# Performance work log

Hardware: AMD Instinct MI355X
Metric: run time of the kernel (lower is better)

Reference implementation:

```python
import jax, jax.numpy as jnp
import numpy as np

B, P, N, S = 32, 16384, 64, 5
BOX_W, SCALE_W, CTX_W, CONF_W = 2.0, 1.0, 1.5, 1.0
BETA = 0.1
REG = 0.1


def _box_iou(a, b):
    # a: [P,4], b: [N,4], boxes are (x1,y1,x2,y2) (torchvision box_iou)
    area_a = (a[:, 2] - a[:, 0]) * (a[:, 3] - a[:, 1])
    area_b = (b[:, 2] - b[:, 0]) * (b[:, 3] - b[:, 1])
    lt = jnp.maximum(a[:, None, :2], b[None, :, :2])
    rb = jnp.minimum(a[:, None, 2:], b[None, :, 2:])
    wh = jnp.maximum(rb - lt, 0.0)
    inter = wh[..., 0] * wh[..., 1]
    return inter / (area_a[:, None] + area_b[None, :] - inter)


def _smooth_l1(x, y, beta=BETA):
    d = jnp.abs(x - y)
    return jnp.where(d < beta, 0.5 * d * d / beta, d - 0.5 * beta)


def _bce_logits(x, y):
    # numerically stable BCEWithLogits, matches torch
    return jnp.maximum(x, 0.0) - x * y + jnp.log1p(jnp.exp(-jnp.abs(x)))


def _per_batch(pscore, pbox, pscale, pctx, tbox, tscale, tctx):
    ious = _box_iou(pbox, tbox)                      # [P, N]
    best_ious = ious.max(axis=0)                     # [N]
    best_idx = ious.argmax(axis=0)                   # [N]
    valid = best_ious > 0.5
    nv = valid.sum()
    denom = jnp.maximum(nv, 1).astype(pbox.dtype)

    # SmoothL1 box loss, weighted by matched IoU, masked mean over valid rows
    sl1 = _smooth_l1(pbox[best_idx], tbox)                          # [N,4]
    box_l = (sl1 * best_ious[:, None] * valid[:, None]).sum() / (denom * 4.0)

    # CrossEntropy over scale classes for matched anchors
    logp = jax.nn.log_softmax(pscale[best_idx], axis=-1)            # [N,S]
    ce = -jnp.take_along_axis(logp, tscale[:, None].astype(jnp.int32), axis=1)[:, 0]
    scale_l = (ce * valid).sum() / denom

    # BCEWithLogits context loss for matched anchors
    bce = _bce_logits(pctx[best_idx], tctx)
    ctx_l = (bce * valid).sum() / denom

    # confidence targets: scatter best IoUs into a zero vector at matched anchors
    Pn = pscore.shape[0]
    idx_safe = jnp.where(valid, best_idx, Pn)
    conf_target = jnp.zeros((Pn + 1,), pscore.dtype).at[idx_safe].max(
        jnp.where(valid, best_ious, 0.0))[:Pn]
    conf_l = _bce_logits(pscore, conf_target).mean()

    # fallback regularization branch (taken when no IoU > 0.5)
    box_reg = jnp.abs(pbox).mean()
    safe = jnp.where(pscale + 1e-6 > 0, pscale + 1e-6, 1.0)
    scale_reg = -(pscale * jnp.log(safe)).mean()
    ctx_reg = jax.nn.softplus(pctx).mean()    # BCEWithLogits vs zeros
    conf_reg = jax.nn.softplus(pscore).mean()

    any_v = nv > 0
    return (jnp.where(any_v, box_l, REG * box_reg),
            jnp.where(any_v, scale_l, REG * scale_reg),
            jnp.where(any_v, ctx_l, REG * ctx_reg),
            jnp.where(any_v, conf_l, conf_reg))


def _forward(pred_scores, pred_boxes, pred_scales, pred_context,
             target_boxes, target_scales, target_context):
    bl, sl, cl, fl = jax.vmap(_per_batch)(
        pred_scores, pred_boxes, pred_scales, pred_context,
        target_boxes, target_scales, target_context)
    box_loss = BOX_W * bl.mean()
    scale_loss = SCALE_W * sl.mean()
    ctx_loss = CTX_W * cl.mean()
    conf_loss = CONF_W * fl.mean()
    total = box_loss + scale_loss + ctx_loss + conf_loss
    return total, box_loss, scale_loss, ctx_loss, conf_loss


def setup_inputs() -> dict:
    key = jax.random.key(0)
    ks = jax.random.split(key, 9)

    def rand_boxes(k, shape):
        xy = jax.random.uniform(k, shape + (2,)) * 0.85
        wh = jax.random.uniform(jax.random.fold_in(k, 1), shape + (2,)) * 0.1 + 0.02
        return jnp.concatenate([xy, xy + wh], axis=-1)

    pred_boxes = rand_boxes(ks[0], (B, P))
    target_boxes = rand_boxes(ks[1], (B, N))
    # plant near-exact matches for half the targets so the IoU>0.5 branch fires
    pred_boxes = pred_boxes.at[:, :N // 2].set(
        target_boxes[:, :N // 2] + 0.002 * jax.random.normal(ks[2], (B, N // 2, 4)))

    return {
        "pred_scores": jax.random.normal(ks[3], (B, P), dtype=jnp.float32),
        "pred_boxes": pred_boxes.astype(jnp.float32),
        "pred_scales": jax.random.normal(ks[4], (B, P, S), dtype=jnp.float32),
        "pred_context": jax.random.normal(ks[5], (B, P), dtype=jnp.float32),
        "target_boxes": target_boxes.astype(jnp.float32),
        "target_scales": jax.random.randint(ks[6], (B, N), 0, S, dtype=jnp.int32),
        "target_context": jax.random.uniform(ks[7], (B, N), dtype=jnp.float32),
        "target_conf": jax.random.uniform(ks[8], (B, P), dtype=jnp.float32),
    }


def reference(pred_scores, pred_boxes, pred_scales, pred_context,
              target_boxes, target_scales, target_context, target_conf):
    # target_conf is read but unused by the original forward; kept for parity
    total, b, s, c, f = _forward(pred_scores, pred_boxes, pred_scales,
                                 pred_context, target_boxes, target_scales,
                                 target_context)
    return jnp.stack([total, b, s, c, f])
```

## Files before the change

kernel.cpp:

```cpp
#include <hip/hip_runtime.h>

#define B_ 32
#define P_ 16384
#define N_ 64
#define S_ 5

constexpr int CHUNKS_A = 32;
constexpr int PRED_PER_BLK_A = P_ / CHUNKS_A;
constexpr int CHUNKS_C = 8;
constexpr int PRED_PER_BLK_C = P_ / CHUNKS_C;

constexpr int ACC_STRIDE = 12;

__device__ __forceinline__ float softplusf_(float x) {
  return fmaxf(x, 0.f) + log1pf(__expf(-fabsf(x)));
}

__global__ __launch_bounds__(256) void kA(const float4* __restrict__ pbox,
                                          const float4* __restrict__ tbox,
                                          unsigned long long* __restrict__ best) {
  __shared__ float sx1[PRED_PER_BLK_A], sy1[PRED_PER_BLK_A],
                   sx2[PRED_PER_BLK_A], sy2[PRED_PER_BLK_A], sar[PRED_PER_BLK_A];
  __shared__ float tg[5][N_];
  const int b = blockIdx.x / CHUNKS_A;
  const int chunk = blockIdx.x % CHUNKS_A;
  const int tid = threadIdx.x;

  if (tid < N_) {
    float4 t = tbox[b * N_ + tid];
    tg[0][tid] = t.x; tg[1][tid] = t.y; tg[2][tid] = t.z; tg[3][tid] = t.w;
    tg[4][tid] = (t.z - t.x) * (t.w - t.y);
  }
  const int base = chunk * PRED_PER_BLK_A;
  for (int i = tid; i < PRED_PER_BLK_A; i += 256) {
    float4 pb = pbox[b * P_ + base + i];
    sx1[i] = pb.x; sy1[i] = pb.y; sx2[i] = pb.z; sy2[i] = pb.w;
    sar[i] = (pb.z - pb.x) * (pb.w - pb.y);
  }
  __syncthreads();

  const int n = tid & 63;
  const int g = tid >> 6;
  const float gx1 = tg[0][n], gy1 = tg[1][n], gx2 = tg[2][n], gy2 = tg[3][n], gar = tg[4][n];

  float bi = -1.f; int bidx = 0;
  const int j0 = g * (PRED_PER_BLK_A / 4);
  #pragma unroll 4
  for (int j = j0; j < j0 + PRED_PER_BLK_A / 4; ++j) {
    float lx = fmaxf(sx1[j], gx1), ly = fmaxf(sy1[j], gy1);
    float rx = fminf(sx2[j], gx2), ry = fminf(sy2[j], gy2);
    float w = fmaxf(rx - lx, 0.f), h = fmaxf(ry - ly, 0.f);
    float inter = w * h;
    float uni = sar[j] + gar - inter;
    float iou = inter * __builtin_amdgcn_rcpf(uni);
    bool upd = iou > bi;
    bi   = upd ? iou : bi;
    bidx = upd ? base + j : bidx;
  }
  unsigned long long packed =
      ((unsigned long long)__float_as_uint(bi) << 32) |
      (unsigned long long)(0xFFFFFFFFu - (unsigned)bidx);
  atomicMax(&best[b * N_ + n], packed);
}

__global__ __launch_bounds__(64) void kB(const unsigned long long* __restrict__ best,
                                         const float* __restrict__ pscore,
                                         const float4* __restrict__ pbox,
                                         const float* __restrict__ pscale,
                                         const float* __restrict__ pctx,
                                         const float4* __restrict__ tbox,
                                         const int* __restrict__ tscale,
                                         const float* __restrict__ tctx,
                                         float* __restrict__ acc) {
  const int b = blockIdx.x, n = threadIdx.x;
  __shared__ float s_iou[N_];
  __shared__ unsigned s_idx[N_];

  unsigned long long pk = best[b * N_ + n];
  float iou = __uint_as_float((unsigned)(pk >> 32));
  unsigned idx = 0xFFFFFFFFu - (unsigned)(pk & 0xFFFFFFFFull);
  bool valid = iou > 0.5f;
  s_iou[n] = iou;
  s_idx[n] = valid ? idx : 0xFFFFFFFFu;
  __syncthreads();

  float boxv = 0.f, scalev = 0.f, ctxv = 0.f, corrv = 0.f;
  float nvv = valid ? 1.f : 0.f;
  if (valid) {
    float4 pb = pbox[b * P_ + idx];
    float4 tb = tbox[b * N_ + n];
    float s1 = 0.f;
    { float d = fabsf(pb.x - tb.x); s1 += (d < 0.1f) ? 5.f * d * d : d - 0.05f; }
    { float d = fabsf(pb.y - tb.y); s1 += (d < 0.1f) ? 5.f * d * d : d - 0.05f; }
    { float d = fabsf(pb.z - tb.z); s1 += (d < 0.1f) ? 5.f * d * d : d - 0.05f; }
    { float d = fabsf(pb.w - tb.w); s1 += (d < 0.1f) ? 5.f * d * d : d - 0.05f; }
    boxv = s1 * iou;

    const float* ps = pscale + (size_t)(b * P_ + idx) * S_;
    float x0 = ps[0], x1 = ps[1], x2 = ps[2], x3 = ps[3], x4 = ps[4];
    float m = fmaxf(fmaxf(fmaxf(x0, x1), fmaxf(x2, x3)), x4);
    float lse = m + logf(expf(x0 - m) + expf(x1 - m) + expf(x2 - m) +
                         expf(x3 - m) + expf(x4 - m));
    int tc = tscale[b * N_ + n];
    scalev = lse - ps[tc];

    float x = pctx[b * P_ + idx], y = tctx[b * N_ + n];
    ctxv = fmaxf(x, 0.f) - x * y + log1pf(expf(-fabsf(x)));

    bool winner = true;
    for (int m2 = 0; m2 < N_; ++m2) {
      if (m2 == n) continue;
      if (s_idx[m2] == idx) {
        float im = s_iou[m2];
        if (im > iou || (im == iou && m2 < n)) winner = false;
      }
    }
    if (winner) corrv = -pscore[b * P_ + idx] * iou;
  }

  for (int o = 32; o; o >>= 1) {
    boxv  += __shfl_down(boxv, o);
    scalev += __shfl_down(scalev, o);
    ctxv  += __shfl_down(ctxv, o);
    corrv += __shfl_down(corrv, o);
    nvv   += __shfl_down(nvv, o);
  }
  if (n == 0) {
    float denom = fmaxf(nvv, 1.f);
    float* a = acc + b * ACC_STRIDE;
    a[0] = boxv / (denom * 4.f);
    a[1] = scalev / denom;
    a[2] = ctxv / denom;
    a[3] = nvv;
    a[4] = corrv;
  }
}

__global__ __launch_bounds__(256) void kC(const float4* __restrict__ pscore4,
                                          const float4* __restrict__ pbox,
                                          const float* __restrict__ pscale,
                                          const float4* __restrict__ pctx4,
                                          float* __restrict__ acc) {
  const int b = blockIdx.x / CHUNKS_C;
  const int chunk = blockIdx.x % CHUNKS_C;
  const int tid = threadIdx.x;
  const bool need_reg = !(acc[b * ACC_STRIDE + 3] > 0.f);
  const int baseP = b * P_ + chunk * PRED_PER_BLK_C;

  float sps = 0.f, boxr = 0.f, scaler = 0.f, ctxr = 0.f;
  for (int i = tid; i < PRED_PER_BLK_C / 4; i += 256) {
    float4 v = pscore4[(baseP >> 2) + i];
    sps += softplusf_(v.x) + softplusf_(v.y) + softplusf_(v.z) + softplusf_(v.w);
  }
  if (need_reg) {
    for (int i = tid; i < PRED_PER_BLK_C; i += 256) {
      float4 t = pbox[baseP + i];
      boxr += fabsf(t.x) + fabsf(t.y) + fabsf(t.z) + fabsf(t.w);
    }
    const float* psc = pscale + (size_t)baseP * S_;
    for (int i = tid; i < PRED_PER_BLK_C * S_; i += 256) {
      float v = psc[i];
      float vp = v + 1e-6f;
      scaler -= v * logf(vp > 0.f ? vp : 1.f);
    }
    for (int i = tid; i < PRED_PER_BLK_C / 4; i += 256) {
      float4 v = pctx4[(baseP >> 2) + i];
      ctxr += softplusf_(v.x) + softplusf_(v.y) + softplusf_(v.z) + softplusf_(v.w);
    }
  }
  for (int o = 32; o; o >>= 1) {
    sps += __shfl_down(sps, o);
    if (need_reg) {
      boxr += __shfl_down(boxr, o);
      scaler += __shfl_down(scaler, o);
      ctxr += __shfl_down(ctxr, o);
    }
  }
  if ((tid & 63) == 0) {
    float* a = acc + b * ACC_STRIDE;
    atomicAdd(&a[5], sps);
    if (need_reg) {
      atomicAdd(&a[6], boxr);
      atomicAdd(&a[7], scaler);
      atomicAdd(&a[8], ctxr);
    }
  }
}

__global__ __launch_bounds__(64) void kD(const float* __restrict__ acc,
                                         float* __restrict__ out) {
  const int t = threadIdx.x;
  float bl = 0.f, sl = 0.f, cl = 0.f, fl = 0.f;
  if (t < B_) {
    const float* a = acc + t * ACC_STRIDE;
    bool anyv = a[3] > 0.f;
    bl = anyv ? a[0] : 0.1f * (a[6] / (float)(P_ * 4));
    sl = anyv ? a[1] : 0.1f * (a[7] / (float)(P_ * S_));
    cl = anyv ? a[2] : 0.1f * (a[8] / (float)P_);
    fl = (a[5] + a[4]) / (float)P_;
  }
  for (int o = 32; o; o >>= 1) {
    bl += __shfl_down(bl, o);
    sl += __shfl_down(sl, o);
    cl += __shfl_down(cl, o);
    fl += __shfl_down(fl, o);
  }
  if (t == 0) {
    float box_loss   = 2.0f * (bl / (float)B_);
    float scale_loss = 1.0f * (sl / (float)B_);
    float ctx_loss   = 1.5f * (cl / (float)B_);
    float conf_loss  = 1.0f * (fl / (float)B_);
    out[0] = box_loss + scale_loss + ctx_loss + conf_loss;
    out[1] = box_loss;
    out[2] = scale_loss;
    out[3] = ctx_loss;
    out[4] = conf_loss;
  }
}

extern "C" void kernel_launch(void* const* d_in, const int* in_sizes, int n_in,
                              void* d_out, int out_size, void* d_ws, size_t ws_size,
                              hipStream_t stream) {
  const float*  pscore = (const float*)d_in[0];
  const float4* pbox   = (const float4*)d_in[1];
  const float*  pscale = (const float*)d_in[2];
  const float*  pctx   = (const float*)d_in[3];
  const float4* tbox   = (const float4*)d_in[4];
  const int*    tscale = (const int*)d_in[5];
  const float*  tctx   = (const float*)d_in[6];

  unsigned long long* best = (unsigned long long*)d_ws;
  float* acc = (float*)((char*)d_ws + (size_t)B_ * N_ * sizeof(unsigned long long));
  size_t zero_bytes = (size_t)B_ * N_ * sizeof(unsigned long long) +
                      (size_t)B_ * ACC_STRIDE * sizeof(float);
  hipMemsetAsync(d_ws, 0, zero_bytes, stream);

  hipLaunchKernelGGL(kA, dim3(B_ * CHUNKS_A), dim3(256), 0, stream, pbox, tbox, best);
  hipLaunchKernelGGL(kB, dim3(B_), dim3(64), 0, stream, best, pscore, pbox, pscale,
                     pctx, tbox, tscale, tctx, acc);
  hipLaunchKernelGGL(kC, dim3(B_ * CHUNKS_C), dim3(256), 0, stream,
                     (const float4*)pscore, pbox, pscale, (const float4*)pctx, acc);
  hipLaunchKernelGGL(kD, dim3(1), dim3(64), 0, stream, acc, (float*)d_out);
}
```

Baseline: 116.5 us.

## Fuse regularization reductions into IoU kernel and replace atomics with per-chunk candidates

The per-anchor reductions (score softplus, box abs, scale entropy, context softplus) move into the IoU kernel, so each block computes them while it already has its 256 anchors loaded, and the separate kC launch goes away. Global atomicMax and atomicAdd are replaced by per-block candidate and partial-sum buffers, merged in kB, which also removes the memset. The regularization terms are now always computed rather than only when a batch has no valid match. The grid grows to 64 chunks per batch, adding more blocks and a wider candidate merge in kB.

```diff
diff --git a/kernel.cpp b/kernel.cpp
--- a/kernel.cpp
+++ b/kernel.cpp
@@ -5,12 +5,10 @@
 #define N_ 64
 #define S_ 5
 
-constexpr int CHUNKS_A = 32;
-constexpr int PRED_PER_BLK_A = P_ / CHUNKS_A;
-constexpr int CHUNKS_C = 8;
-constexpr int PRED_PER_BLK_C = P_ / CHUNKS_C;
-
+constexpr int CHUNKS = 64;
+constexpr int PRED_PER_BLK = P_ / CHUNKS;
 constexpr int ACC_STRIDE = 12;
+
 
 __device__ __forceinline__ float softplusf_(float x) {
   return fmaxf(x, 0.f) + log1pf(__expf(-fabsf(x)));
@@ -18,52 +16,92 @@
 
 __global__ __launch_bounds__(256) void kA(const float4* __restrict__ pbox,
                                           const float4* __restrict__ tbox,
-                                          unsigned long long* __restrict__ best) {
-  __shared__ float sx1[PRED_PER_BLK_A], sy1[PRED_PER_BLK_A],
-                   sx2[PRED_PER_BLK_A], sy2[PRED_PER_BLK_A], sar[PRED_PER_BLK_A];
-  __shared__ float tg[5][N_];
-  const int b = blockIdx.x / CHUNKS_A;
-  const int chunk = blockIdx.x % CHUNKS_A;
-  const int tid = threadIdx.x;
+                                          const float* __restrict__ pscore,
+                                          const float* __restrict__ pscale,
+                                          const float* __restrict__ pctx,
+                                          unsigned long long* __restrict__ cand,
+                                          float4* __restrict__ partial) {
+  __shared__ float4 sbox[PRED_PER_BLK];
+  __shared__ float  sar[PRED_PER_BLK];
+  __shared__ float  tg[5][N_];
+  __shared__ unsigned long long merge[4][N_];
+  __shared__ float  red[4][4];
+
+  const int b     = blockIdx.x / CHUNKS;
+  const int chunk = blockIdx.x % CHUNKS;
+  const int tid   = threadIdx.x;
+  const int base  = chunk * PRED_PER_BLK;
+  const int gbase = b * P_ + base;
 
   if (tid < N_) {
     float4 t = tbox[b * N_ + tid];
     tg[0][tid] = t.x; tg[1][tid] = t.y; tg[2][tid] = t.z; tg[3][tid] = t.w;
     tg[4][tid] = (t.z - t.x) * (t.w - t.y);
   }
-  const int base = chunk * PRED_PER_BLK_A;
-  for (int i = tid; i < PRED_PER_BLK_A; i += 256) {
-    float4 pb = pbox[b * P_ + base + i];
-    sx1[i] = pb.x; sy1[i] = pb.y; sx2[i] = pb.z; sy2[i] = pb.w;
-    sar[i] = (pb.z - pb.x) * (pb.w - pb.y);
+  float4 pb = pbox[gbase + tid];
+  sbox[tid] = pb;
+  sar[tid]  = (pb.z - pb.x) * (pb.w - pb.y);
+  float boxr = fabsf(pb.x) + fabsf(pb.y) + fabsf(pb.z) + fabsf(pb.w);
+  float sps  = softplusf_(pscore[gbase + tid]);
+  float ctxr = softplusf_(pctx[gbase + tid]);
+  float scaler = 0.f;
+  const float* psc = pscale + (size_t)gbase * S_;
+  #pragma unroll
+  for (int i = 0; i < S_; ++i) {
+    float v  = psc[tid + i * 256];
+    float vp = v + 1e-6f;
+    scaler  -= v * logf(vp > 0.f ? vp : 1.f);
   }
   __syncthreads();
 
   const int n = tid & 63;
   const int g = tid >> 6;
-  const float gx1 = tg[0][n], gy1 = tg[1][n], gx2 = tg[2][n], gy2 = tg[3][n], gar = tg[4][n];
-
-  float bi = -1.f; int bidx = 0;
-  const int j0 = g * (PRED_PER_BLK_A / 4);
+  const float gx1 = tg[0][n], gy1 = tg[1][n], gx2 = tg[2][n], gy2 = tg[3][n],
+              gar = tg[4][n];
+
+  float bi = -1.f; int bj = 0;
+  const int j0 = g * (PRED_PER_BLK / 4);
   #pragma unroll 4
-  for (int j = j0; j < j0 + PRED_PER_BLK_A / 4; ++j) {
-    float lx = fmaxf(sx1[j], gx1), ly = fmaxf(sy1[j], gy1);
-    float rx = fminf(sx2[j], gx2), ry = fminf(sy2[j], gy2);
-    float w = fmaxf(rx - lx, 0.f), h = fmaxf(ry - ly, 0.f);
+  for (int j = j0; j < j0 + PRED_PER_BLK / 4; ++j) {
+    float4 q  = sbox[j];
+    float su  = sar[j] + gar;
+    float w   = fmaxf(fminf(q.z, gx2) - fmaxf(q.x, gx1), 0.f);
+    float h   = fmaxf(fminf(q.w, gy2) - fmaxf(q.y, gy1), 0.f);
     float inter = w * h;
-    float uni = sar[j] + gar - inter;
-    float iou = inter * __builtin_amdgcn_rcpf(uni);
-    bool upd = iou > bi;
-    bi   = upd ? iou : bi;
-    bidx = upd ? base + j : bidx;
-  }
-  unsigned long long packed =
-      ((unsigned long long)__float_as_uint(bi) << 32) |
-      (unsigned long long)(0xFFFFFFFFu - (unsigned)bidx);
-  atomicMax(&best[b * N_ + n], packed);
-}
-
-__global__ __launch_bounds__(64) void kB(const unsigned long long* __restrict__ best,
+    float iou = inter * __builtin_amdgcn_rcpf(su - inter);
+    bool upd  = iou > bi;
+    bi = upd ? iou : bi;
+    bj = upd ? j : bj;
+  }
+  merge[g][n] = ((unsigned long long)__float_as_uint(bi) << 32) |
+                (unsigned long long)(0xFFFFFFFFu - (unsigned)(base + bj));
+
+  float p0 = sps, p1 = boxr, p2 = scaler, p3 = ctxr;
+  for (int o = 32; o; o >>= 1) {
+    p0 += __shfl_down(p0, o); p1 += __shfl_down(p1, o);
+    p2 += __shfl_down(p2, o); p3 += __shfl_down(p3, o);
+  }
+  if (n == 0) { red[g][0] = p0; red[g][1] = p1; red[g][2] = p2; red[g][3] = p3; }
+  __syncthreads();
+
+  if (tid < N_) {
+    unsigned long long m = merge[0][tid];
+    unsigned long long v1 = merge[1][tid]; m = v1 > m ? v1 : m;
+    unsigned long long v2 = merge[2][tid]; m = v2 > m ? v2 : m;
+    unsigned long long v3 = merge[3][tid]; m = v3 > m ? v3 : m;
+    cand[(size_t)blockIdx.x * N_ + tid] = m;
+  }
+  if (tid == 64) {
+    partial[blockIdx.x] =
+        make_float4(red[0][0] + red[1][0] + red[2][0] + red[3][0],
+                    red[0][1] + red[1][1] + red[2][1] + red[3][1],
+                    red[0][2] + red[1][2] + red[2][2] + red[3][2],
+                    red[0][3] + red[1][3] + red[2][3] + red[3][3]);
+  }
+}
+
+__global__ __launch_bounds__(64) void kB(const unsigned long long* __restrict__ cand,
+                                         const float4* __restrict__ partial,
                                          const float* __restrict__ pscore,
                                          const float4* __restrict__ pbox,
                                          const float* __restrict__ pscale,
@@ -76,7 +114,14 @@
   __shared__ float s_iou[N_];
   __shared__ unsigned s_idx[N_];
 
-  unsigned long long pk = best[b * N_ + n];
+  unsigned long long pk = 0ull;
+  const unsigned long long* cb = cand + (size_t)b * CHUNKS * N_ + n;
+  #pragma unroll 8
+  for (int c = 0; c < CHUNKS; ++c) {
+    unsigned long long v = cb[(size_t)c * N_];
+    pk = v > pk ? v : pk;
+  }
+
   float iou = __uint_as_float((unsigned)(pk >> 32));
   unsigned idx = 0xFFFFFFFFu - (unsigned)(pk & 0xFFFFFFFFull);
   bool valid = iou > 0.5f;
@@ -125,6 +170,16 @@
     corrv += __shfl_down(corrv, o);
     nvv   += __shfl_down(nvv, o);
   }
+
+  float4 pp = partial[b * CHUNKS + n];
+  float sps = pp.x, boxr = pp.y, scaler = pp.z, ctxr = pp.w;
+  for (int o = 32; o; o >>= 1) {
+    sps += __shfl_down(sps, o);
+    boxr += __shfl_down(boxr, o);
+    scaler += __shfl_down(scaler, o);
+    ctxr += __shfl_down(ctxr, o);
+  }
+
   if (n == 0) {
     float denom = fmaxf(nvv, 1.f);
     float* a = acc + b * ACC_STRIDE;
@@ -133,57 +188,10 @@
     a[2] = ctxv / denom;
     a[3] = nvv;
     a[4] = corrv;
-  }
-}
-
-__global__ __launch_bounds__(256) void kC(const float4* __restrict__ pscore4,
-                                          const float4* __restrict__ pbox,
-                                          const float* __restrict__ pscale,
-                                          const float4* __restrict__ pctx4,
-                                          float* __restrict__ acc) {
-  const int b = blockIdx.x / CHUNKS_C;
-  const int chunk = blockIdx.x % CHUNKS_C;
-  const int tid = threadIdx.x;
-  const bool need_reg = !(acc[b * ACC_STRIDE + 3] > 0.f);
-  const int baseP = b * P_ + chunk * PRED_PER_BLK_C;
-
-  float sps = 0.f, boxr = 0.f, scaler = 0.f, ctxr = 0.f;
-  for (int i = tid; i < PRED_PER_BLK_C / 4; i += 256) {
-    float4 v = pscore4[(baseP >> 2) + i];
-    sps += softplusf_(v.x) + softplusf_(v.y) + softplusf_(v.z) + softplusf_(v.w);
-  }
-  if (need_reg) {
-    for (int i = tid; i < PRED_PER_BLK_C; i += 256) {
-      float4 t = pbox[baseP + i];
-      boxr += fabsf(t.x) + fabsf(t.y) + fabsf(t.z) + fabsf(t.w);
-    }
-    const float* psc = pscale + (size_t)baseP * S_;
-    for (int i = tid; i < PRED_PER_BLK_C * S_; i += 256) {
-      float v = psc[i];
-      float vp = v + 1e-6f;
-      scaler -= v * logf(vp > 0.f ? vp : 1.f);
-    }
-    for (int i = tid; i < PRED_PER_BLK_C / 4; i += 256) {
-      float4 v = pctx4[(baseP >> 2) + i];
-      ctxr += softplusf_(v.x) + softplusf_(v.y) + softplusf_(v.z) + softplusf_(v.w);
-    }
-  }
-  for (int o = 32; o; o >>= 1) {
-    sps += __shfl_down(sps, o);
-    if (need_reg) {
-      boxr += __shfl_down(boxr, o);
-      scaler += __shfl_down(scaler, o);
-      ctxr += __shfl_down(ctxr, o);
-    }
-  }
-  if ((tid & 63) == 0) {
-    float* a = acc + b * ACC_STRIDE;
-    atomicAdd(&a[5], sps);
-    if (need_reg) {
-      atomicAdd(&a[6], boxr);
-      atomicAdd(&a[7], scaler);
-      atomicAdd(&a[8], ctxr);
-    }
+    a[5] = sps;
+    a[6] = boxr;
+    a[7] = scaler;
+    a[8] = ctxr;
   }
 }
 
@@ -229,16 +237,13 @@
   const int*    tscale = (const int*)d_in[5];
   const float*  tctx   = (const float*)d_in[6];
 
-  unsigned long long* best = (unsigned long long*)d_ws;
-  float* acc = (float*)((char*)d_ws + (size_t)B_ * N_ * sizeof(unsigned long long));
-  size_t zero_bytes = (size_t)B_ * N_ * sizeof(unsigned long long) +
-                      (size_t)B_ * ACC_STRIDE * sizeof(float);
-  hipMemsetAsync(d_ws, 0, zero_bytes, stream);
-
-  hipLaunchKernelGGL(kA, dim3(B_ * CHUNKS_A), dim3(256), 0, stream, pbox, tbox, best);
-  hipLaunchKernelGGL(kB, dim3(B_), dim3(64), 0, stream, best, pscore, pbox, pscale,
-                     pctx, tbox, tscale, tctx, acc);
-  hipLaunchKernelGGL(kC, dim3(B_ * CHUNKS_C), dim3(256), 0, stream,
-                     (const float4*)pscore, pbox, pscale, (const float4*)pctx, acc);
+  unsigned long long* cand = (unsigned long long*)d_ws;
+  float4* partial = (float4*)((char*)d_ws + (size_t)B_ * CHUNKS * N_ * 8);
+  float* acc = (float*)((char*)partial + (size_t)B_ * CHUNKS * sizeof(float4));
+
+  hipLaunchKernelGGL(kA, dim3(B_ * CHUNKS), dim3(256), 0, stream,
+                     pbox, tbox, pscore, pscale, pctx, cand, partial);
+  hipLaunchKernelGGL(kB, dim3(B_), dim3(64), 0, stream, cand, partial, pscore,
+                     pbox, pscale, pctx, tbox, tscale, tctx, acc);
   hipLaunchKernelGGL(kD, dim3(1), dim3(64), 0, stream, acc, (float*)d_out);
 }
```

Measured after the change: 117.7 us, median of 2. About the same (+1.1%).
